# Optimization experiments

Measured on AMD Instinct MI355X. Metric: run time of the kernel, lower is better.

Reference implementation:

```python
import jax, jax.numpy as jnp
import numpy as np
from jax.scipy.special import logsumexp

B, D, T, O = 8, 64, 512, 256  # batch, channels (d_dim), observed timestamps, grid points


def setup_inputs() -> dict:
    key = jax.random.key(0)
    k1, k2, k3 = jax.random.split(key, 3)
    vals = jax.random.normal(k1, (B, D, T), dtype=jnp.float32)
    mask = (jax.random.uniform(k2, (B, D, T)) < 0.7).astype(jnp.float32)
    mask = mask.at[:, :, 0].set(1.0)  # ensure >=1 observation per (b, channel)
    times = jnp.sort(jax.random.uniform(k3, (B, D, T), dtype=jnp.float32), axis=-1)
    x = jnp.concatenate([vals, mask, times], axis=1)  # (B, 3*D, T)
    grid = jnp.broadcast_to(jnp.linspace(0.0, 1.0, O, dtype=jnp.float32), (B, O))
    kernel = jnp.zeros((D,), dtype=jnp.float32)  # learned per-channel log-bandwidth
    return {"x": x, "interpolation_grid": grid, "kernel": kernel}


def reference(x, interpolation_grid, kernel):
    d_dim = kernel.shape[0]
    x_t = x[:, :d_dim]            # (B, D, T) observed values
    m = x[:, d_dim:2 * d_dim]     # (B, D, T) observation mask in {0,1}
    t = x[:, 2 * d_dim:3 * d_dim] # (B, D, T) observation timestamps

    alpha = jax.nn.softplus(kernel)[None, :, None, None]  # pos_kernel, (1,D,1,1)
    # squared distance between observed times and reference grid: (B,D,T,O)
    norm = (t[:, :, :, None] - interpolation_grid[:, None, None, :]) ** 2
    # log(mask): -inf (clamped) where unobserved, 0 where observed
    logm = jnp.log(jnp.maximum(m, 1e-30))[:, :, :, None]

    s = -alpha * norm + logm                      # (B,D,T,O) masked RBF logits
    w = logsumexp(s, axis=2)                      # (B,D,O) intensity channel
    w1 = jnp.exp(s - w[:, :, None, :])            # softmax over T
    y = jnp.sum(w1 * x_t[:, :, :, None], axis=2)  # (B,D,O) smooth interpolation

    s10 = -10.0 * alpha * norm + logm             # sharper kernel (transient)
    wt_lse = logsumexp(s10, axis=2)
    wt = jnp.exp(s10 - wt_lse[:, :, None, :])
    y_trans = jnp.sum(wt * x_t[:, :, :, None], axis=2)  # (B,D,O)

    return jnp.concatenate([y, w, y_trans], axis=1)  # (B, 3*D, O)
```

## Files before the change

### kernel.cpp

```cpp
#include <hip/hip_runtime.h>
#include <math.h>


namespace {
constexpr int kB = 8, kD = 64, kT = 512, kO = 256;
constexpr int kTH = 512;
constexpr float kLOG2E = 1.4426950408889634f;
constexpr float kLN2   = 0.6931471805599453f;
constexpr float kLM    = 99.65784284662087f;
}

__device__ __forceinline__ float2 pkfma(float2 a, float b, float2 c) {
    return make_float2(fmaf(a.x, b, c.x), fmaf(a.y, b, c.y));
}
__device__ __forceinline__ float2 pkadd(float2 a, float2 b) {
    return make_float2(a.x + b.x, a.y + b.y);
}

__global__ __launch_bounds__(kTH, 4) void interp_kernel(
    const float* __restrict__ x,
    const float* __restrict__ grid,
    const float* __restrict__ kern,
    float* __restrict__ out)
{
    __shared__ __align__(16) float smem[4096 + 8];
    float* s_u   = smem;
    float* s_w   = smem + kT;
    float* s_v   = smem + 2 * kT;
    float* s_cnt = smem + 4096;

    const int tid  = threadIdx.x;
    const int lane = tid & 63;
    const int wv   = tid >> 6;
    const int ow   = wv & 1;
    const int tq   = wv >> 1;
    const int o0   = ow * 128 + lane;
    const int o1   = o0 + 64;

    const int bd = blockIdx.x;
    const int b  = bd >> 6;
    const int d  = bd & (kD - 1);

    const float* base = x + (size_t)b * (3 * kD * kT);
    const float* Vrow = base + (size_t)d * kT;
    const float* Mrow = base + (size_t)(kD + d) * kT;
    const float* Trow = base + (size_t)(2 * kD + d) * kT;

    const float k     = kern[d];
    const float alpha = fmaxf(k, 0.0f) + log1pf(expf(-fabsf(k)));
    const float a2    = alpha * kLOG2E;

    const float tt = Trow[tid];
    const float mm = Mrow[tid];
    const float vv = Vrow[tid];
    const bool keep = (mm != 0.0f);
    const unsigned long long ball = __ballot(keep);
    if (lane == 0) s_cnt[wv] = (float)__popcll(ball);
    __syncthreads();

    int bsum = 0, total = 0;
    #pragma unroll
    for (int j = 0; j < 8; ++j) {
        const int c = (int)s_cnt[j];
        bsum  += (j < wv) ? c : 0;
        total += c;
    }
    const int padded = (total + 15) & ~15;

    if (keep) {
        const int pos = bsum + __popcll(ball & ((1ull << lane) - 1ull));
        s_u[pos] = fmaf(-a2 * tt, tt, 0.0f);
        s_w[pos] = 2.0f * a2 * tt;
        s_v[pos] = vv;
    }
    if (tid >= total && tid < padded) {
        s_u[tid] = -500.0f;
        s_w[tid] = 0.0f;
        s_v[tid] = 0.0f;
    }
    __syncthreads();

    const float g0 = grid[b * kO + o0];
    const float g1 = grid[b * kO + o1];
    const float2 cc = make_float2(-a2 * g0 * g0, -a2 * g1 * g1);

    float2 acc_l = make_float2(0.f, 0.f), acc_y = make_float2(0.f, 0.f);
    float2 acc_q = make_float2(0.f, 0.f), acc_z = make_float2(0.f, 0.f);

    const int chunk = padded >> 2;
    const int t0 = tq * chunk;
    for (int t = t0; t < t0 + chunk; t += 4) {
        const float4 uu = *(const float4*)(s_u + t);
        const float4 ww = *(const float4*)(s_w + t);
        const float4 vs = *(const float4*)(s_v + t);

        #pragma unroll
        for (int j = 0; j < 4; ++j) {
            const float u = (&uu.x)[j], w = (&ww.x)[j], v = (&vs.x)[j];
            const float2 a = pkadd(pkfma(make_float2(g0, g1), w,
                                         make_float2(u, u)), cc);
            const float2 e = make_float2(__builtin_amdgcn_exp2f(a.x),
                                         __builtin_amdgcn_exp2f(a.y));
            const float2 E = make_float2(__builtin_amdgcn_exp2f(10.0f * a.x),
                                         __builtin_amdgcn_exp2f(10.0f * a.y));
            acc_l = pkadd(acc_l, e);
            acc_y = pkfma(e, v, acc_y);
            acc_q = pkadd(acc_q, E);
            acc_z = pkfma(E, v, acc_z);
        }
    }

    __syncthreads();
    float (*sp)[4][kO] = (float (*)[4][kO])smem;
    sp[tq][0][o0] = acc_l.x;  sp[tq][0][o1] = acc_l.y;
    sp[tq][1][o0] = acc_y.x;  sp[tq][1][o1] = acc_y.y;
    sp[tq][2][o0] = acc_q.x;  sp[tq][2][o1] = acc_q.y;
    sp[tq][3][o0] = acc_z.x;  sp[tq][3][o1] = acc_z.y;
    __syncthreads();

    if (tq == 0) {
        float L0=0.f,L1=0.f, Y0=0.f,Y1=0.f, Q0=0.f,Q1=0.f, Z0=0.f,Z1=0.f;
        #pragma unroll
        for (int j = 0; j < 4; ++j) {
            L0 += sp[j][0][o0]; Y0 += sp[j][1][o0];
            Q0 += sp[j][2][o0]; Z0 += sp[j][3][o0];
            L1 += sp[j][0][o1]; Y1 += sp[j][1][o1];
            Q1 += sp[j][2][o1]; Z1 += sp[j][3][o1];
        }
        const float w0o = __builtin_amdgcn_logf(L0) * kLN2;
        const float w1o = __builtin_amdgcn_logf(L1) * kLN2;
        float* ob = out + (size_t)b * (3 * kD * kO);
        ob[(size_t)d * kO + o0]            = Y0 / L0;
        ob[(size_t)d * kO + o1]            = Y1 / L1;
        ob[(size_t)(kD + d) * kO + o0]     = w0o;
        ob[(size_t)(kD + d) * kO + o1]     = w1o;
        ob[(size_t)(2 * kD + d) * kO + o0] = Z0 / Q0;
        ob[(size_t)(2 * kD + d) * kO + o1] = Z1 / Q1;
    }
}

extern "C" void kernel_launch(void* const* d_in, const int* in_sizes, int n_in,
                              void* d_out, int out_size, void* d_ws, size_t ws_size,
                              hipStream_t stream) {
    const float* x    = (const float*)d_in[0];
    const float* grid = (const float*)d_in[1];
    const float* kern = (const float*)d_in[2];
    float* out        = (float*)d_out;
    interp_kernel<<<dim3(kB * kD), dim3(kTH), 0, stream>>>(x, grid, kern, out);
}
```

Before: 71.34 us.

## Derive grid-shifted exponentials by multiplying precomputed ratios instead of exp2 per point

Assumes a uniform grid and computes exp2 only for the first 64 grid points. The other three 64-point blocks come from multiplying by a per-timestamp ratio exp2(w*h64) precomputed in shared memory. The sharp kernel is taken as P^10 through repeated squaring rather than a second exp2, and the -a2*g^2 term is folded out of the sums and into the log at the end. This cuts transcendental work by about 8x, but it relies on a linearly spaced grid and risks overflow or underflow in the ratio products and P^10. T is now split across all 8 waves, and the cross-wave reduction is changed to match.

```diff
diff --git a/kernel.cpp b/kernel.cpp
--- a/kernel.cpp
+++ b/kernel.cpp
@@ -7,15 +7,9 @@
 constexpr int kTH = 512;
 constexpr float kLOG2E = 1.4426950408889634f;
 constexpr float kLN2   = 0.6931471805599453f;
-constexpr float kLM    = 99.65784284662087f;
 }
 
-__device__ __forceinline__ float2 pkfma(float2 a, float b, float2 c) {
-    return make_float2(fmaf(a.x, b, c.x), fmaf(a.y, b, c.y));
-}
-__device__ __forceinline__ float2 pkadd(float2 a, float2 b) {
-    return make_float2(a.x + b.x, a.y + b.y);
-}
+typedef float f2 __attribute__((ext_vector_type(2)));
 
 __global__ __launch_bounds__(kTH, 4) void interp_kernel(
     const float* __restrict__ x,
@@ -23,19 +17,13 @@
     const float* __restrict__ kern,
     float* __restrict__ out)
 {
-    __shared__ __align__(16) float smem[4096 + 8];
-    float* s_u   = smem;
-    float* s_w   = smem + kT;
-    float* s_v   = smem + 2 * kT;
-    float* s_cnt = smem + 4096;
+    __shared__ __align__(16) float smem[8192 + 8];
+    float* s_v   = smem + 2048;
+    float* s_cnt = smem + 8192;
 
     const int tid  = threadIdx.x;
     const int lane = tid & 63;
     const int wv   = tid >> 6;
-    const int ow   = wv & 1;
-    const int tq   = wv >> 1;
-    const int o0   = ow * 128 + lane;
-    const int o1   = o0 + 64;
 
     const int bd = blockIdx.x;
     const int b  = bd >> 6;
@@ -49,6 +37,9 @@
     const float k     = kern[d];
     const float alpha = fmaxf(k, 0.0f) + log1pf(expf(-fabsf(k)));
     const float a2    = alpha * kLOG2E;
+
+    const float* gB  = grid + b * kO;
+    const float h64  = (gB[kO - 1] - gB[0]) * (64.0f / 255.0f);
 
     const float tt = Trow[tid];
     const float mm = Mrow[tid];
@@ -65,77 +56,78 @@
         bsum  += (j < wv) ? c : 0;
         total += c;
     }
-    const int padded = (total + 15) & ~15;
+    const int padded = (total + 31) & ~31;
 
     if (keep) {
         const int pos = bsum + __popcll(ball & ((1ull << lane) - 1ull));
-        s_u[pos] = fmaf(-a2 * tt, tt, 0.0f);
-        s_w[pos] = 2.0f * a2 * tt;
+        const float u  = -a2 * tt * tt;
+        const float w  = 2.0f * a2 * tt;
+        const float wh = w * h64;
+        ((float4*)smem)[pos] = make_float4(u, w,
+            __builtin_amdgcn_exp2f(wh),
+            __builtin_amdgcn_exp2f(10.0f * wh));
         s_v[pos] = vv;
     }
     if (tid >= total && tid < padded) {
-        s_u[tid] = -500.0f;
-        s_w[tid] = 0.0f;
+        ((float4*)smem)[tid] = make_float4(-500.0f, 0.0f, 1.0f, 1.0f);
         s_v[tid] = 0.0f;
     }
     __syncthreads();
 
-    const float g0 = grid[b * kO + o0];
-    const float g1 = grid[b * kO + o1];
-    const float2 cc = make_float2(-a2 * g0 * g0, -a2 * g1 * g1);
+    const float g0 = gB[lane];
 
-    float2 acc_l = make_float2(0.f, 0.f), acc_y = make_float2(0.f, 0.f);
-    float2 acc_q = make_float2(0.f, 0.f), acc_z = make_float2(0.f, 0.f);
+    f2 aL0 = {0.f, 0.f}, aY0 = {0.f, 0.f};
+    f2 aL1 = {0.f, 0.f}, aY1 = {0.f, 0.f};
+    f2 aL2 = {0.f, 0.f}, aY2 = {0.f, 0.f};
+    f2 aL3 = {0.f, 0.f}, aY3 = {0.f, 0.f};
 
-    const int chunk = padded >> 2;
-    const int t0 = tq * chunk;
+    const int chunk = padded >> 3;
+    const int t0 = wv * chunk;
     for (int t = t0; t < t0 + chunk; t += 4) {
-        const float4 uu = *(const float4*)(s_u + t);
-        const float4 ww = *(const float4*)(s_w + t);
-        const float4 vs = *(const float4*)(s_v + t);
-
         #pragma unroll
-        for (int j = 0; j < 4; ++j) {
-            const float u = (&uu.x)[j], w = (&ww.x)[j], v = (&vs.x)[j];
-            const float2 a = pkadd(pkfma(make_float2(g0, g1), w,
-                                         make_float2(u, u)), cc);
-            const float2 e = make_float2(__builtin_amdgcn_exp2f(a.x),
-                                         __builtin_amdgcn_exp2f(a.y));
-            const float2 E = make_float2(__builtin_amdgcn_exp2f(10.0f * a.x),
-                                         __builtin_amdgcn_exp2f(10.0f * a.y));
-            acc_l = pkadd(acc_l, e);
-            acc_y = pkfma(e, v, acc_y);
-            acc_q = pkadd(acc_q, E);
-            acc_z = pkfma(E, v, acc_z);
+        for (int ss = 0; ss < 4; ++ss) {
+            const float4 f = ((const float4*)smem)[t + ss];
+            const float  va = s_v[t + ss];
+            const float a0 = fmaf(f.y, g0, f.x);
+            const float P  = __builtin_amdgcn_exp2f(a0);
+            const float P2 = P * P, P4 = P2 * P2, P8 = P4 * P4;
+            f2 pq;  pq.x  = P;    pq.y  = P8 * P2;
+            f2 rho; rho.x = f.z;  rho.y = f.w;
+            f2 vva; vva.x = va;   vva.y = va;
+            aL0 += pq; aY0 += pq * vva; pq *= rho;
+            aL1 += pq; aY1 += pq * vva; pq *= rho;
+            aL2 += pq; aY2 += pq * vva; pq *= rho;
+            aL3 += pq; aY3 += pq * vva;
         }
     }
 
     __syncthreads();
-    float (*sp)[4][kO] = (float (*)[4][kO])smem;
-    sp[tq][0][o0] = acc_l.x;  sp[tq][0][o1] = acc_l.y;
-    sp[tq][1][o0] = acc_y.x;  sp[tq][1][o1] = acc_y.y;
-    sp[tq][2][o0] = acc_q.x;  sp[tq][2][o1] = acc_q.y;
-    sp[tq][3][o0] = acc_z.x;  sp[tq][3][o1] = acc_z.y;
+    float4* part = (float4*)smem;
+    part[wv * kO + lane      ] = make_float4(aL0.x, aY0.x, aL0.y, aY0.y);
+    part[wv * kO + lane +  64] = make_float4(aL1.x, aY1.x, aL1.y, aY1.y);
+    part[wv * kO + lane + 128] = make_float4(aL2.x, aY2.x, aL2.y, aY2.y);
+    part[wv * kO + lane + 192] = make_float4(aL3.x, aY3.x, aL3.y, aY3.y);
     __syncthreads();
 
-    if (tq == 0) {
-        float L0=0.f,L1=0.f, Y0=0.f,Y1=0.f, Q0=0.f,Q1=0.f, Z0=0.f,Z1=0.f;
-        #pragma unroll
-        for (int j = 0; j < 4; ++j) {
-            L0 += sp[j][0][o0]; Y0 += sp[j][1][o0];
-            Q0 += sp[j][2][o0]; Z0 += sp[j][3][o0];
-            L1 += sp[j][0][o1]; Y1 += sp[j][1][o1];
-            Q1 += sp[j][2][o1]; Z1 += sp[j][3][o1];
-        }
-        const float w0o = __builtin_amdgcn_logf(L0) * kLN2;
-        const float w1o = __builtin_amdgcn_logf(L1) * kLN2;
-        float* ob = out + (size_t)b * (3 * kD * kO);
-        ob[(size_t)d * kO + o0]            = Y0 / L0;
-        ob[(size_t)d * kO + o1]            = Y1 / L1;
-        ob[(size_t)(kD + d) * kO + o0]     = w0o;
-        ob[(size_t)(kD + d) * kO + o1]     = w1o;
-        ob[(size_t)(2 * kD + d) * kO + o0] = Z0 / Q0;
-        ob[(size_t)(2 * kD + d) * kO + o1] = Z1 / Q1;
+    const int o     = tid & 255;
+    const int which = tid >> 8;
+    const float* pb = smem + o * 4 + which * 2;
+    f2 s2 = {0.f, 0.f};
+    #pragma unroll
+    for (int j = 0; j < 8; ++j) {
+        const f2 p = *(const f2*)(pb + j * 1024);
+        s2 += p;
+    }
+
+    float* ob = out + (size_t)b * (3 * kD * kO);
+    if (which == 0) {
+        const float L = s2.x, Y = s2.y;
+        const float gv = gB[o];
+        ob[(size_t)d * kO + o] = Y / L;
+        ob[(size_t)(kD + d) * kO + o] =
+            (__builtin_amdgcn_logf(L) - a2 * gv * gv) * kLN2;
+    } else {
+        ob[(size_t)(2 * kD + d) * kO + o] = s2.y / s2.x;
     }
 }
 
```

Measured after the change: 67.61 us. 1.06x faster.
